# Kernel tuning notes

Measured on AMD Instinct MI355X. Metric: run time of the kernel, lower is better.

## Reference

```python
import jax, jax.numpy as jnp
import numpy as np

IN_FEATURES = 1024
BATCH = 65536


def setup_inputs() -> dict:
    key = jax.random.key(0)
    ks = jax.random.split(key, 7)
    return {
        "x": jax.random.normal(ks[0], (BATCH, IN_FEATURES), dtype=jnp.float32),
        "W": jax.random.normal(ks[1], (IN_FEATURES, IN_FEATURES), dtype=jnp.float32),
        "P": jax.random.normal(ks[2], (IN_FEATURES,), dtype=jnp.float32),
        "w": jax.random.normal(ks[3], (1,), dtype=jnp.float32),
        "p": jax.random.normal(ks[4], (1,), dtype=jnp.float32),
        "sine_w": jax.random.normal(ks[5], (1,), dtype=jnp.float32),
        "cosine_w": jax.random.normal(ks[6], (1,), dtype=jnp.float32),
    }


def reference(x, W, P, w, p, sine_w, cosine_w):
    # Time2Vec: linear term + periodic (sin/cos mixed) term, concatenated.
    original = w * x + p                      # [B, F]
    z = jnp.matmul(x, W) + P                  # [B, F]
    periodic = sine_w * jnp.sin(z) + cosine_w * jnp.cos(z)  # [B, F]
    return jnp.concatenate((original, periodic), axis=-1)    # [B, 2F]
```

## Files before the change

kernel.cpp:

```cpp
#include <hip/hip_runtime.h>


typedef __attribute__((ext_vector_type(4))) float    f32x4;
typedef __attribute__((ext_vector_type(8))) short    short8;
typedef __attribute__((ext_vector_type(4))) unsigned short u16x4;

#define IN_F   1024
#define BATCH  65536

__device__ __forceinline__ unsigned short f2bf(float f) {
    unsigned u = __float_as_uint(f);
    u += 0x7fffu + ((u >> 16) & 1u);
    return (unsigned short)(u >> 16);
}
__device__ __forceinline__ float bf2f(unsigned short b) {
    return __uint_as_float(((unsigned)b) << 16);
}

__device__ __forceinline__ void async_copy16(const void* g, void* l) {
    __builtin_amdgcn_global_load_lds(
        (const __attribute__((address_space(1))) void*)g,
        (__attribute__((address_space(3))) void*)l, 16, 0, 0);
}

__global__ __launch_bounds__(256) void prep_x_kernel(
    const f32x4* __restrict__ x4, const float* __restrict__ wp,
    const float* __restrict__ pp, float* __restrict__ out,
    u16x4* __restrict__ Xhi, u16x4* __restrict__ Xlo)
{
    unsigned idx = blockIdx.x * 256u + threadIdx.x;
    f32x4 v = x4[idx];
    float w = wp[0], p = pp[0];
    unsigned e = idx * 4u;
    unsigned r = e >> 10, cc = e & 1023u;
    f32x4 o = v * w + p;
    *(f32x4*)(out + (size_t)r * 2048 + cc) = o;
    u16x4 h, l;
#pragma unroll
    for (int i = 0; i < 4; ++i) {
        unsigned short hh = f2bf(v[i]);
        h[i] = hh;
        l[i] = f2bf(v[i] - bf2f(hh));
    }
    Xhi[idx] = h;
    Xlo[idx] = l;
}

__global__ __launch_bounds__(256) void prep_w_kernel(
    const float* __restrict__ W,
    unsigned short* __restrict__ Whi, unsigned short* __restrict__ Wlo)
{
    __shared__ float t[32][33];
    int tx = threadIdx.x, ty = threadIdx.y;
    int n0 = blockIdx.x * 32, k0 = blockIdx.y * 32;
#pragma unroll
    for (int i = 0; i < 4; ++i)
        t[ty + i * 8][tx] = W[(size_t)(k0 + ty + i * 8) * IN_F + n0 + tx];
    __syncthreads();
#pragma unroll
    for (int i = 0; i < 4; ++i) {
        float v = t[tx][ty + i * 8];
        int n = n0 + ty + i * 8, k = k0 + tx;
        unsigned short h = f2bf(v);
        Whi[(size_t)n * IN_F + k] = h;
        Wlo[(size_t)n * IN_F + k] = f2bf(v - bf2f(h));
    }
}

__global__ __launch_bounds__(512, 2) void gemm_kernel(
    const unsigned short* __restrict__ Xhi, const unsigned short* __restrict__ Xlo,
    const unsigned short* __restrict__ Whi, const unsigned short* __restrict__ Wlo,
    const float* __restrict__ P, const float* __restrict__ swp,
    const float* __restrict__ cwp, float* __restrict__ out)
{
    __shared__ __align__(16) char As[65536];
    __shared__ __align__(16) char Bs[65536];

    const int tid  = threadIdx.x;
    const int lane = tid & 63;
    const int wave = tid >> 6;
    const int wm   = wave >> 2;
    const int wn   = wave & 3;

    int bid = blockIdx.x;
    int wg  = (bid & 7) * 128 + (bid >> 3);
    const int m0 = (wg >> 2) * 256;
    const int n0 = (wg & 3) * 256;

    const int fr    = lane & 15;
    const int fsw   = (fr ^ (fr >> 2)) & 3;
    const int slotp = (lane >> 4) ^ fsw;
    const unsigned aoff = (unsigned)((wm * 128 + fr) * 64 + slotp * 16);
    const unsigned boff = (unsigned)((wn * 64 + fr) * 64 + slotp * 16);

    const int srow  = tid >> 2;
    const int sslot = (tid & 3) ^ (((tid >> 2) ^ (tid >> 4)) & 3);
    const size_t aRow0 = (size_t)(m0 + srow) * IN_F + sslot * 8;
    const size_t aRow1 = (size_t)(m0 + 128 + srow) * IN_F + sslot * 8;
    const size_t bRow0 = (size_t)(n0 + srow) * IN_F + sslot * 8;
    const size_t bRow1 = (size_t)(n0 + 128 + srow) * IN_F + sslot * 8;
    const unsigned ldsW = (unsigned)(wave * 1024);

    f32x4 acc[8][4] = {};

    auto stageA = [&](int kt) {
        const unsigned short* Ap = ((kt >> 5) == 2) ? Xlo : Xhi;
        int k0e = (kt & 31) * 32;
        char* d = As + (kt & 3) * 16384 + ldsW;
        async_copy16(Ap + aRow0 + k0e, d);
        async_copy16(Ap + aRow1 + k0e, d + 8192);
    };
    auto stageB = [&](int kt) {
        const unsigned short* Bp = ((kt >> 5) == 1) ? Wlo : Whi;
        int k0e = (kt & 31) * 32;
        char* d = Bs + (kt & 3) * 16384 + ldsW;
        async_copy16(Bp + bRow0 + k0e, d);
        async_copy16(Bp + bRow1 + k0e, d + 8192);
    };

    stageA(0); stageB(0);
    stageA(1); stageB(1);
    stageA(2); stageB(2);
    asm volatile("s_waitcnt vmcnt(8)" ::: "memory");
    __builtin_amdgcn_s_barrier();

    for (int t = 0; t < 96; ++t) {
        const char* aBase = As + (t & 3) * 16384 + aoff;
        const char* bBase = Bs + (t & 3) * 16384 + boff;
        short8 av[4], bv[4], av2[4];

#pragma unroll
        for (int i = 0; i < 4; ++i) av[i] = *(const short8*)(aBase + i * 1024);
#pragma unroll
        for (int j = 0; j < 4; ++j) bv[j] = *(const short8*)(bBase + j * 1024);
        if (t + 3 < 96) stageA(t + 3);
        __builtin_amdgcn_s_barrier();
        __builtin_amdgcn_s_setprio(1);
#pragma unroll
        for (int i = 0; i < 4; ++i)
#pragma unroll
            for (int j = 0; j < 4; ++j)
                acc[i][j] = __builtin_amdgcn_mfma_f32_16x16x32_bf16(
                    av[i], bv[j], acc[i][j], 0, 0, 0);
        __builtin_amdgcn_s_setprio(0);
        __builtin_amdgcn_s_barrier();

#pragma unroll
        for (int i = 0; i < 4; ++i) av2[i] = *(const short8*)(aBase + 4096 + i * 1024);
        if (t + 3 < 96) stageB(t + 3);
        __builtin_amdgcn_s_barrier();
        __builtin_amdgcn_s_setprio(1);
#pragma unroll
        for (int i = 0; i < 4; ++i)
#pragma unroll
            for (int j = 0; j < 4; ++j)
                acc[4 + i][j] = __builtin_amdgcn_mfma_f32_16x16x32_bf16(
                    av2[i], bv[j], acc[4 + i][j], 0, 0, 0);
        __builtin_amdgcn_s_setprio(0);
        if (t < 93) { asm volatile("s_waitcnt vmcnt(8)" ::: "memory"); }
        else        { asm volatile("s_waitcnt vmcnt(0)" ::: "memory"); }
        __builtin_amdgcn_s_barrier();
    }

    const float sw = swp[0], cw = cwp[0];
#pragma unroll
    for (int j = 0; j < 4; ++j) {
        const int colg = n0 + wn * 64 + j * 16 + fr;
        const float pcol = P[colg];
#pragma unroll
        for (int i = 0; i < 8; ++i) {
#pragma unroll
            for (int r = 0; r < 4; ++r) {
                int rowg = m0 + wm * 128 + i * 16 + (lane >> 4) * 4 + r;
                float z = acc[i][j][r] + pcol;
                float val = sw * __sinf(z) + cw * __cosf(z);
                out[(size_t)rowg * 2048 + 1024 + colg] = val;
            }
        }
    }
}

__global__ __launch_bounds__(256) void naive_kernel(
    const float* __restrict__ x, const float* __restrict__ W,
    const float* __restrict__ P, const float* __restrict__ wp,
    const float* __restrict__ pp, const float* __restrict__ swp,
    const float* __restrict__ cwp, float* __restrict__ out)
{
    size_t idx = (size_t)blockIdx.x * 256 + threadIdx.x;
    if (idx >= (size_t)BATCH * IN_F) return;
    size_t r = idx >> 10;
    int n = (int)(idx & 1023);
    float acc = 0.f;
    for (int k = 0; k < IN_F; ++k)
        acc = fmaf(x[r * IN_F + k], W[(size_t)k * IN_F + n], acc);
    float z = acc + P[n];
    out[r * 2048 + n] = wp[0] * x[r * IN_F + n] + pp[0];
    out[r * 2048 + 1024 + n] = swp[0] * __sinf(z) + cwp[0] * __cosf(z);
}

extern "C" void kernel_launch(void* const* d_in, const int* in_sizes, int n_in,
                              void* d_out, int out_size, void* d_ws, size_t ws_size,
                              hipStream_t stream)
{
    const float* x   = (const float*)d_in[0];
    const float* W   = (const float*)d_in[1];
    const float* P   = (const float*)d_in[2];
    const float* w   = (const float*)d_in[3];
    const float* p   = (const float*)d_in[4];
    const float* swv = (const float*)d_in[5];
    const float* cwv = (const float*)d_in[6];
    float* out = (float*)d_out;

    const size_t xElems = (size_t)BATCH * IN_F;
    const size_t wElems = (size_t)IN_F * IN_F;
    const size_t need   = xElems * 2 * 2 + wElems * 2 * 2;

    if (ws_size >= need) {
        unsigned short* Xhi = (unsigned short*)d_ws;
        unsigned short* Xlo = Xhi + xElems;
        unsigned short* Whi = Xlo + xElems;
        unsigned short* Wlo = Whi + wElems;

        prep_x_kernel<<<65536, 256, 0, stream>>>(
            (const f32x4*)x, w, p, out, (u16x4*)Xhi, (u16x4*)Xlo);
        prep_w_kernel<<<dim3(32, 32), dim3(32, 8), 0, stream>>>(W, Whi, Wlo);
        gemm_kernel<<<1024, 512, 0, stream>>>(Xhi, Xlo, Whi, Wlo, P, swv, cwv, out);
    } else {
        naive_kernel<<<(unsigned)((xElems + 255) / 256), 256, 0, stream>>>(
            x, W, P, w, p, swv, cwv, out);
    }
}
```

Measured before the change: 1.161 ms.

## Switch GEMM to 32x32x16 MFMA with register double-buffered LDS reads

The GEMM inner loop now uses 32x32x16 bf16 MFMA instead of 16x16x32, which means fewer, larger matrix instructions and fewer LDS fragment reads per FLOP. The main loop is unrolled by two with ping-pong register fragments, so LDS reads for the next k-tile overlap the current MFMAs, and A/B staging is merged into one call with a single barrier per tile. The prep_x kernel also becomes a grid-stride loop over 2048 blocks. In exchange there is higher register pressure from the 16-wide accumulators and double fragments, and the epilogue store pattern changes.

```diff
diff --git a/kernel.cpp b/kernel.cpp
--- a/kernel.cpp
+++ b/kernel.cpp
@@ -1,9 +1,10 @@
 #include <hip/hip_runtime.h>
 
 
-typedef __attribute__((ext_vector_type(4))) float    f32x4;
-typedef __attribute__((ext_vector_type(8))) short    short8;
-typedef __attribute__((ext_vector_type(4))) unsigned short u16x4;
+typedef __attribute__((ext_vector_type(4)))  float    f32x4;
+typedef __attribute__((ext_vector_type(16))) float    f32x16;
+typedef __attribute__((ext_vector_type(8)))  short    short8;
+typedef __attribute__((ext_vector_type(4)))  unsigned short u16x4;
 
 #define IN_F   1024
 #define BATCH  65536
@@ -28,22 +29,24 @@
     const float* __restrict__ pp, float* __restrict__ out,
     u16x4* __restrict__ Xhi, u16x4* __restrict__ Xlo)
 {
-    unsigned idx = blockIdx.x * 256u + threadIdx.x;
-    f32x4 v = x4[idx];
-    float w = wp[0], p = pp[0];
-    unsigned e = idx * 4u;
-    unsigned r = e >> 10, cc = e & 1023u;
-    f32x4 o = v * w + p;
-    *(f32x4*)(out + (size_t)r * 2048 + cc) = o;
-    u16x4 h, l;
-#pragma unroll
-    for (int i = 0; i < 4; ++i) {
-        unsigned short hh = f2bf(v[i]);
-        h[i] = hh;
-        l[i] = f2bf(v[i] - bf2f(hh));
-    }
-    Xhi[idx] = h;
-    Xlo[idx] = l;
+    const float w = wp[0], p = pp[0];
+    for (unsigned idx = blockIdx.x * 256u + threadIdx.x; idx < 16777216u;
+         idx += 2048u * 256u) {
+        f32x4 v = x4[idx];
+        unsigned e = idx * 4u;
+        unsigned r = e >> 10, cc = e & 1023u;
+        f32x4 o = v * w + p;
+        *(f32x4*)(out + (size_t)r * 2048 + cc) = o;
+        u16x4 h, l;
+#pragma unroll
+        for (int i = 0; i < 4; ++i) {
+            unsigned short hh = f2bf(v[i]);
+            h[i] = hh;
+            l[i] = f2bf(v[i] - bf2f(hh));
+        }
+        Xhi[idx] = h;
+        Xlo[idx] = l;
+    }
 }
 
 __global__ __launch_bounds__(256) void prep_w_kernel(
@@ -67,6 +70,35 @@
     }
 }
 
+
+#define READS(tt, A_, B_) do {                                               \
+    const char* aT_ = As + ((tt) & 3) * 16384;                               \
+    const char* bT_ = Bs + ((tt) & 3) * 16384;                               \
+    A_[0] = *(const short8*)(aT_ + aO0);        A_[1] = *(const short8*)(aT_ + aO1);        \
+    A_[2] = *(const short8*)(aT_ + aO0 + 2048); A_[3] = *(const short8*)(aT_ + aO1 + 2048); \
+    A_[4] = *(const short8*)(aT_ + aO0 + 4096); A_[5] = *(const short8*)(aT_ + aO1 + 4096); \
+    A_[6] = *(const short8*)(aT_ + aO0 + 6144); A_[7] = *(const short8*)(aT_ + aO1 + 6144); \
+    B_[0] = *(const short8*)(bT_ + bO0);        B_[1] = *(const short8*)(bT_ + bO1);        \
+    B_[2] = *(const short8*)(bT_ + bO0 + 2048); B_[3] = *(const short8*)(bT_ + bO1 + 2048); \
+} while (0)
+
+#define MFMAS(A_, B_) do {                                                   \
+    __builtin_amdgcn_s_setprio(1);                                           \
+    _Pragma("unroll")                                                        \
+    for (int mi_ = 0; mi_ < 4; ++mi_)                                        \
+        _Pragma("unroll")                                                    \
+        for (int nj_ = 0; nj_ < 2; ++nj_)                                    \
+            acc[mi_][nj_] = __builtin_amdgcn_mfma_f32_32x32x16_bf16(         \
+                A_[mi_ * 2 + 0], B_[nj_ * 2 + 0], acc[mi_][nj_], 0, 0, 0);   \
+    _Pragma("unroll")                                                        \
+    for (int mi_ = 0; mi_ < 4; ++mi_)                                        \
+        _Pragma("unroll")                                                    \
+        for (int nj_ = 0; nj_ < 2; ++nj_)                                    \
+            acc[mi_][nj_] = __builtin_amdgcn_mfma_f32_32x32x16_bf16(         \
+                A_[mi_ * 2 + 1], B_[nj_ * 2 + 1], acc[mi_][nj_], 0, 0, 0);   \
+    __builtin_amdgcn_s_setprio(0);                                           \
+} while (0)
+
 __global__ __launch_bounds__(512, 2) void gemm_kernel(
     const unsigned short* __restrict__ Xhi, const unsigned short* __restrict__ Xlo,
     const unsigned short* __restrict__ Whi, const unsigned short* __restrict__ Wlo,
@@ -87,11 +119,14 @@
     const int m0 = (wg >> 2) * 256;
     const int n0 = (wg & 3) * 256;
 
-    const int fr    = lane & 15;
-    const int fsw   = (fr ^ (fr >> 2)) & 3;
-    const int slotp = (lane >> 4) ^ fsw;
-    const unsigned aoff = (unsigned)((wm * 128 + fr) * 64 + slotp * 16);
-    const unsigned boff = (unsigned)((wn * 64 + fr) * 64 + slotp * 16);
+    const int rl  = lane & 31;
+    const int kh  = lane >> 5;
+    const int fsw = (rl ^ (rl >> 2)) & 3;
+    const int s0  = kh ^ fsw;
+    const unsigned aO0 = (unsigned)((wm * 128 + rl) * 64 + s0 * 16);
+    const unsigned aO1 = aO0 ^ 32u;
+    const unsigned bO0 = (unsigned)((wn * 64 + rl) * 64 + s0 * 16);
+    const unsigned bO1 = bO0 ^ 32u;
 
     const int srow  = tid >> 2;
     const int sslot = (tid & 3) ^ (((tid >> 2) ^ (tid >> 4)) & 3);
@@ -101,80 +136,66 @@
     const size_t bRow1 = (size_t)(n0 + 128 + srow) * IN_F + sslot * 8;
     const unsigned ldsW = (unsigned)(wave * 1024);
 
-    f32x4 acc[8][4] = {};
-
-    auto stageA = [&](int kt) {
+    f32x16 acc[4][2] = {};
+
+    auto stage = [&](int kt) {
         const unsigned short* Ap = ((kt >> 5) == 2) ? Xlo : Xhi;
-        int k0e = (kt & 31) * 32;
-        char* d = As + (kt & 3) * 16384 + ldsW;
-        async_copy16(Ap + aRow0 + k0e, d);
-        async_copy16(Ap + aRow1 + k0e, d + 8192);
-    };
-    auto stageB = [&](int kt) {
         const unsigned short* Bp = ((kt >> 5) == 1) ? Wlo : Whi;
         int k0e = (kt & 31) * 32;
-        char* d = Bs + (kt & 3) * 16384 + ldsW;
-        async_copy16(Bp + bRow0 + k0e, d);
-        async_copy16(Bp + bRow1 + k0e, d + 8192);
+        char* dA = As + (kt & 3) * 16384 + ldsW;
+        char* dB = Bs + (kt & 3) * 16384 + ldsW;
+        async_copy16(Ap + aRow0 + k0e, dA);
+        async_copy16(Ap + aRow1 + k0e, dA + 8192);
+        async_copy16(Bp + bRow0 + k0e, dB);
+        async_copy16(Bp + bRow1 + k0e, dB + 8192);
     };
 
-    stageA(0); stageB(0);
-    stageA(1); stageB(1);
-    stageA(2); stageB(2);
-    asm volatile("s_waitcnt vmcnt(8)" ::: "memory");
+    stage(0); stage(1); stage(2);
+    asm volatile("s_waitcnt vmcnt(4)" ::: "memory");
     __builtin_amdgcn_s_barrier();
 
-    for (int t = 0; t < 96; ++t) {
-        const char* aBase = As + (t & 3) * 16384 + aoff;
-        const char* bBase = Bs + (t & 3) * 16384 + boff;
-        short8 av[4], bv[4], av2[4];
-
-#pragma unroll
-        for (int i = 0; i < 4; ++i) av[i] = *(const short8*)(aBase + i * 1024);
-#pragma unroll
-        for (int j = 0; j < 4; ++j) bv[j] = *(const short8*)(bBase + j * 1024);
-        if (t + 3 < 96) stageA(t + 3);
+    short8 fA0[8], fB0[4], fA1[8], fB1[4];
+    READS(0, fA0, fB0);
+
+    for (int t = 0; t < 92; t += 2) {
+        READS(t + 1, fA1, fB1);
+        stage(t + 3);
+        MFMAS(fA0, fB0);
+        asm volatile("s_waitcnt vmcnt(4)" ::: "memory");
         __builtin_amdgcn_s_barrier();
-        __builtin_amdgcn_s_setprio(1);
-#pragma unroll
-        for (int i = 0; i < 4; ++i)
-#pragma unroll
-            for (int j = 0; j < 4; ++j)
-                acc[i][j] = __builtin_amdgcn_mfma_f32_16x16x32_bf16(
-                    av[i], bv[j], acc[i][j], 0, 0, 0);
-        __builtin_amdgcn_s_setprio(0);
+        READS(t + 2, fA0, fB0);
+        stage(t + 4);
+        MFMAS(fA1, fB1);
+        asm volatile("s_waitcnt vmcnt(4)" ::: "memory");
         __builtin_amdgcn_s_barrier();
-
-#pragma unroll
-        for (int i = 0; i < 4; ++i) av2[i] = *(const short8*)(aBase + 4096 + i * 1024);
-        if (t + 3 < 96) stageB(t + 3);
-        __builtin_amdgcn_s_barrier();
-        __builtin_amdgcn_s_setprio(1);
-#pragma unroll
-        for (int i = 0; i < 4; ++i)
-#pragma unroll
-            for (int j = 0; j < 4; ++j)
-                acc[4 + i][j] = __builtin_amdgcn_mfma_f32_16x16x32_bf16(
-                    av2[i], bv[j], acc[4 + i][j], 0, 0, 0);
-        __builtin_amdgcn_s_setprio(0);
-        if (t < 93) { asm volatile("s_waitcnt vmcnt(8)" ::: "memory"); }
-        else        { asm volatile("s_waitcnt vmcnt(0)" ::: "memory"); }
-        __builtin_amdgcn_s_barrier();
-    }
+    }
+    READS(93, fA1, fB1);
+    stage(95);
+    MFMAS(fA0, fB0);
+    asm volatile("s_waitcnt vmcnt(4)" ::: "memory");
+    __builtin_amdgcn_s_barrier();
+
+    READS(94, fA0, fB0);
+    MFMAS(fA1, fB1);
+    asm volatile("s_waitcnt vmcnt(0)" ::: "memory");
+    __builtin_amdgcn_s_barrier();
+
+    READS(95, fA1, fB1);
+    MFMAS(fA0, fB0);
+    MFMAS(fA1, fB1);
 
     const float sw = swp[0], cw = cwp[0];
 #pragma unroll
-    for (int j = 0; j < 4; ++j) {
-        const int colg = n0 + wn * 64 + j * 16 + fr;
+    for (int nj = 0; nj < 2; ++nj) {
+        const int colg = n0 + wn * 64 + nj * 32 + rl;
         const float pcol = P[colg];
 #pragma unroll
-        for (int i = 0; i < 8; ++i) {
-#pragma unroll
-            for (int r = 0; r < 4; ++r) {
-                int rowg = m0 + wm * 128 + i * 16 + (lane >> 4) * 4 + r;
-                float z = acc[i][j][r] + pcol;
-                float val = sw * __sinf(z) + cw * __cosf(z);
-                out[(size_t)rowg * 2048 + 1024 + colg] = val;
+        for (int mi = 0; mi < 4; ++mi) {
+#pragma unroll
+            for (int r = 0; r < 16; ++r) {
+                int rowg = m0 + wm * 128 + mi * 32 + (r & 3) + 8 * (r >> 2) + 4 * kh;
+                float z = acc[mi][nj][r] + pcol;
+                out[(size_t)rowg * 2048 + 1024 + colg] = sw * __sinf(z) + cw * __cosf(z);
             }
         }
     }
@@ -221,7 +242,7 @@
         unsigned short* Whi = Xlo + xElems;
         unsigned short* Wlo = Whi + wElems;
 
-        prep_x_kernel<<<65536, 256, 0, stream>>>(
+        prep_x_kernel<<<2048, 256, 0, stream>>>(
             (const f32x4*)x, w, p, out, (u16x4*)Xhi, (u16x4*)Xlo);
         prep_w_kernel<<<dim3(32, 32), dim3(32, 8), 0, stream>>>(W, Whi, Wlo);
         gemm_kernel<<<1024, 512, 0, stream>>>(Xhi, Xlo, Whi, Wlo, P, swv, cwv, out);
```

New measurement: 1.129 ms. -2.7%, faster.
